# Kernel optimization log

Hardware: AMD Instinct MI355X
Metric: run time of the kernel (lower is better)

The kernel has to match this reference:

```python
import jax, jax.numpy as jnp
import numpy as np

D_MODEL = 1024
NUM_EXPERTS = 64
TOP_K = 2
TEMPERATURE = 1.0


def setup_inputs() -> dict:
    key = jax.random.key(0)
    k1, k2, k3, k4 = jax.random.split(key, 4)
    mh_output = jax.random.normal(k1, (8, 4096, D_MODEL), dtype=jnp.float32)
    noise = jax.random.normal(k2, (8, 4096, NUM_EXPERTS), dtype=jnp.float32)  # randn_like sample, externalized
    # nn.Linear weights: shape [out, in], init normal(0, 0.02); biases zero
    W_route = jax.random.normal(k3, (NUM_EXPERTS, D_MODEL), dtype=jnp.float32) * 0.02
    b_route = jnp.zeros((NUM_EXPERTS,), dtype=jnp.float32)
    W_noise = jax.random.normal(k4, (NUM_EXPERTS, D_MODEL), dtype=jnp.float32) * 0.02
    b_noise = jnp.zeros((NUM_EXPERTS,), dtype=jnp.float32)
    return {"mh_output": mh_output, "noise": noise, "W_route": W_route,
            "b_route": b_route, "W_noise": W_noise, "b_noise": b_noise}


def reference(mh_output, noise, W_route, b_route, W_noise, b_noise):
    # logits = topkroute_linear(mh_output); noise_logits = noise_linear(mh_output)
    logits = jnp.einsum('bsd,ed->bse', mh_output, W_route) + b_route
    noise_logits = jnp.einsum('bsd,ed->bse', mh_output, W_noise) + b_noise
    # noisy logits = logits + temperature * randn * softplus(noise_logits)
    noisy = logits + TEMPERATURE * noise * jax.nn.softplus(noise_logits)
    # top-k, scatter into -inf, softmax  ==  softmax over top-k values scattered into zeros
    top_vals, indices = jax.lax.top_k(noisy, TOP_K)          # [b, s, k]
    probs_k = jax.nn.softmax(top_vals, axis=-1)              # softmax(-inf elsewhere) -> 0 elsewhere
    one_hot = jax.nn.one_hot(indices, NUM_EXPERTS, dtype=noisy.dtype)  # [b, s, k, E]
    router_output = jnp.sum(one_hot * probs_k[..., None], axis=-2)     # [b, s, E]
    return router_output, indices
```

## Files before the change

### kernel.cpp

```cpp
#include <hip/hip_runtime.h>
#include <hip/hip_bf16.h>
#include <math.h>


#define T_TOKENS 32768
#define D_MODEL  1024
#define NE       64
#define NCOL     128
#define M_TILE   64
#define NCHUNK   32
#define CS_LD    68
#define OUT_IDX_BASE ((size_t)T_TOKENS * NE)
#define W_ELEMS  (NCOL * D_MODEL)

typedef short  bf16x8  __attribute__((ext_vector_type(8)));
typedef float  floatx4 __attribute__((ext_vector_type(4)));

__device__ __forceinline__ float softplus_f(float x) {
    return fmaxf(x, 0.f) + log1pf(expf(-fabsf(x)));
}

__device__ __forceinline__ void cvt8(const float4 a, const float4 b,
                                     int4* hi, int4* lo) {
    float v[8] = {a.x, a.y, a.z, a.w, b.x, b.y, b.z, b.w};
    int hw[4], lw[4];
    #pragma unroll
    for (int p = 0; p < 4; ++p) {
        float2 f2 = make_float2(v[2 * p], v[2 * p + 1]);
        __hip_bfloat162 h2 = __float22bfloat162_rn(f2);
        int u; __builtin_memcpy(&u, &h2, 4);
        float h0 = __uint_as_float(((unsigned)u) << 16);
        float h1 = __uint_as_float(((unsigned)u) & 0xFFFF0000u);
        float2 l2 = make_float2(v[2 * p] - h0, v[2 * p + 1] - h1);
        __hip_bfloat162 L2 = __float22bfloat162_rn(l2);
        int ul; __builtin_memcpy(&ul, &L2, 4);
        hw[p] = u; lw[p] = ul;
    }
    *hi = make_int4(hw[0], hw[1], hw[2], hw[3]);
    *lo = make_int4(lw[0], lw[1], lw[2], lw[3]);
}

__global__ __launch_bounds__(256) void prepack_w(
    const float* __restrict__ Wr, const float* __restrict__ Wn,
    short* __restrict__ Bh, short* __restrict__ Bl)
{
    int g   = blockIdx.x * 256 + threadIdx.x;
    int n   = g & 15;
    int kg  = (g >> 4) & 127;
    int t2  = g >> 11;
    int col = t2 * 16 + n;
    const float* src = (col < NE ? Wr + (size_t)col * D_MODEL
                                 : Wn + (size_t)(col - NE) * D_MODEL) + kg * 8;
    float4 a = *(const float4*)src;
    float4 b = *(const float4*)(src + 4);
    int4 hi, lo;
    cvt8(a, b, &hi, &lo);
    *(int4*)(Bh + (size_t)g * 8) = hi;
    *(int4*)(Bl + (size_t)g * 8) = lo;
}

__global__ __launch_bounds__(256, 2) void router_mfma(
    const float* __restrict__ A,
    const float* __restrict__ noise,
    const float* __restrict__ br,
    const float* __restrict__ bn,
    const short* __restrict__ Bh,
    const short* __restrict__ Bl,
    float* __restrict__ out)
{
    __shared__ __align__(16) short Ah[2][M_TILE * 32];
    __shared__ __align__(16) short Al[2][M_TILE * 32];
    __shared__ float Cs[M_TILE * CS_LD];
    __shared__ float s_p1[M_TILE], s_p2[M_TILE];
    __shared__ int   s_e1[M_TILE], s_e2[M_TILE];

    const int tid  = threadIdx.x;
    const int lane = tid & 63;
    const int wid  = tid >> 6;
    const int n16  = lane & 15;
    const int quad = lane >> 4;
    const int m0   = blockIdx.x * M_TILE;

    const int r  = tid & 63;
    const int kh = tid >> 6;
    const float* pA = A + (size_t)(m0 + r) * D_MODEL + kh * 8;
    const int sBase = (kh * M_TILE + r) * 8;

    const int bBaseR = ((wid * 128 + quad) * 16 + n16) * 8;
    const int bBaseN = (((4 + wid) * 128 + quad) * 16 + n16) * 8;

    floatx4 acc[4][2];
    #pragma unroll
    for (int i = 0; i < 4; ++i) { acc[i][0] = (floatx4)0.f; acc[i][1] = (floatx4)0.f; }

    {
        float4 a0 = *(const float4*)pA;
        float4 a1 = *(const float4*)(pA + 4);
        int4 hi, lo;
        cvt8(a0, a1, &hi, &lo);
        *(int4*)&Ah[0][sBase] = hi;
        *(int4*)&Al[0][sBase] = lo;
    }
    bf16x8 bhR, blR, bhN, blN;
    bhR = *(const bf16x8*)(Bh + bBaseR);
    blR = *(const bf16x8*)(Bl + bBaseR);
    bhN = *(const bf16x8*)(Bh + bBaseN);
    blN = *(const bf16x8*)(Bl + bBaseN);
    float4 aP1a = *(const float4*)(pA + 32), aP1b = *(const float4*)(pA + 36);
    float4 aP2a = *(const float4*)(pA + 64), aP2b = *(const float4*)(pA + 68);
    __syncthreads();

    for (int kc = 0; kc < NCHUNK; ++kc) {
        const int cur = kc & 1, nxt = cur ^ 1;

        float4 f0, f1;
        if (kc + 3 < NCHUNK) {
            f0 = *(const float4*)(pA + (kc + 3) * 32);
            f1 = *(const float4*)(pA + (kc + 3) * 32 + 4);
        }
        bf16x8 bhRn, blRn, bhNn, blNn;
        if (kc + 1 < NCHUNK) {
            int o = (kc + 1) * 512;
            bhRn = *(const bf16x8*)(Bh + bBaseR + o);
            blRn = *(const bf16x8*)(Bl + bBaseR + o);
            bhNn = *(const bf16x8*)(Bh + bBaseN + o);
            blNn = *(const bf16x8*)(Bl + bBaseN + o);
        }

        bf16x8 afh[4], afl[4];
        #pragma unroll
        for (int mf = 0; mf < 4; ++mf) {
            int g = (quad * M_TILE + mf * 16 + n16) * 8;
            afh[mf] = *(const bf16x8*)&Ah[cur][g];
            afl[mf] = *(const bf16x8*)&Al[cur][g];
        }

        if (kc + 1 < NCHUNK) {
            int4 hi, lo;
            cvt8(aP1a, aP1b, &hi, &lo);
            *(int4*)&Ah[nxt][sBase] = hi;
            *(int4*)&Al[nxt][sBase] = lo;
        }

        #pragma unroll
        for (int mf = 0; mf < 4; ++mf) {
            acc[mf][0] = __builtin_amdgcn_mfma_f32_16x16x32_bf16(afh[mf], bhR, acc[mf][0], 0, 0, 0);
            acc[mf][0] = __builtin_amdgcn_mfma_f32_16x16x32_bf16(afh[mf], blR, acc[mf][0], 0, 0, 0);
            acc[mf][0] = __builtin_amdgcn_mfma_f32_16x16x32_bf16(afl[mf], bhR, acc[mf][0], 0, 0, 0);
            acc[mf][1] = __builtin_amdgcn_mfma_f32_16x16x32_bf16(afh[mf], bhN, acc[mf][1], 0, 0, 0);
            acc[mf][1] = __builtin_amdgcn_mfma_f32_16x16x32_bf16(afh[mf], blN, acc[mf][1], 0, 0, 0);
            acc[mf][1] = __builtin_amdgcn_mfma_f32_16x16x32_bf16(afl[mf], blN == blN ? bhN : bhN, acc[mf][1], 0, 0, 0);
        }

        __syncthreads();

        aP1a = aP2a; aP1b = aP2b; aP2a = f0; aP2b = f1;
        bhR = bhRn; blR = blRn; bhN = bhNn; blN = blNn;
    }

    {
        int e = wid * 16 + n16;
        float brv = br[e], bnv = bn[e];
        #pragma unroll
        for (int mf = 0; mf < 4; ++mf)
            #pragma unroll
            for (int rr = 0; rr < 4; ++rr) {
                int t = mf * 16 + quad * 4 + rr;
                float nz    = noise[(size_t)(m0 + t) * NE + e];
                float route = acc[mf][0][rr] + brv;
                float nl    = acc[mf][1][rr] + bnv;
                Cs[t * CS_LD + e] = fmaf(nz, softplus_f(nl), route);
            }
    }
    __syncthreads();

    if (tid < M_TILE) {
        const int t = tid;
        float v1 = -INFINITY, v2 = -INFINITY;
        int e1 = 0, e2 = 0;
        #pragma unroll
        for (int e4 = 0; e4 < 16; ++e4) {
            float4 q = *(const float4*)&Cs[t * CS_LD + e4 * 4];
            float qa[4] = {q.x, q.y, q.z, q.w};
            #pragma unroll
            for (int c = 0; c < 4; ++c) {
                float v = qa[c];
                int e = e4 * 4 + c;
                if (v > v1) { v2 = v1; e2 = e1; v1 = v; e1 = e; }
                else if (v > v2) { v2 = v; e2 = e; }
            }
        }
        float ex = expf(v2 - v1);
        float denom = 1.f + ex;
        s_p1[t] = 1.f / denom;
        s_p2[t] = ex / denom;
        s_e1[t] = e1;
        s_e2[t] = e2;
        float2 iv = make_float2((float)e1, (float)e2);
        *(float2*)(out + OUT_IDX_BASE + (size_t)(m0 + t) * 2) = iv;
    }
    __syncthreads();

    #pragma unroll
    for (int i = 0; i < 4; ++i) {
        int gi = i * 256 + tid;
        int t  = gi >> 4;
        int e0 = (gi & 15) * 4;
        float p1 = s_p1[t], p2 = s_p2[t];
        int   e1 = s_e1[t], e2 = s_e2[t];
        float4 v;
        v.x = (e0 + 0 == e1) ? p1 : ((e0 + 0 == e2) ? p2 : 0.f);
        v.y = (e0 + 1 == e1) ? p1 : ((e0 + 1 == e2) ? p2 : 0.f);
        v.z = (e0 + 2 == e1) ? p1 : ((e0 + 2 == e2) ? p2 : 0.f);
        v.w = (e0 + 3 == e1) ? p1 : ((e0 + 3 == e2) ? p2 : 0.f);
        *(float4*)(out + (size_t)(m0 + t) * NE + e0) = v;
    }
}

extern "C" void kernel_launch(void* const* d_in, const int* in_sizes, int n_in,
                              void* d_out, int out_size, void* d_ws, size_t ws_size,
                              hipStream_t stream) {
    const float* A     = (const float*)d_in[0];
    const float* noise = (const float*)d_in[1];
    const float* Wr    = (const float*)d_in[2];
    const float* br    = (const float*)d_in[3];
    const float* Wn    = (const float*)d_in[4];
    const float* bn    = (const float*)d_in[5];
    float* out = (float*)d_out;

    short* Bh = (short*)d_ws;
    short* Bl = Bh + W_ELEMS;

    prepack_w<<<dim3(W_ELEMS / 8 / 256), dim3(256), 0, stream>>>(Wr, Wn, Bh, Bl);
    router_mfma<<<dim3(T_TOKENS / M_TILE), dim3(256), 0, stream>>>(A, noise, br, bn, Bh, Bl, out);
}
```

Baseline: 229.3 us.

## Load A fragments directly into registers, dropping LDS staging and loop barriers

Each wave now converts its own A rows from global memory straight into MFMA fragments instead of staging hi/lo bf16 tiles in shared memory. The block's warps are re-split into a 2x2 grid over tokens and columns, so each wave covers 32 tokens by 64 columns. This removes the per-chunk LDS writes, reads and __syncthreads, and drops the min-2-blocks launch bound. The cost is that each A element is loaded and converted by two waves, and more B fragments are held in registers, which raises register pressure and can lower occupancy.

```diff
diff --git a/kernel.cpp b/kernel.cpp
--- a/kernel.cpp
+++ b/kernel.cpp
@@ -20,8 +20,8 @@
     return fmaxf(x, 0.f) + log1pf(expf(-fabsf(x)));
 }
 
-__device__ __forceinline__ void cvt8(const float4 a, const float4 b,
-                                     int4* hi, int4* lo) {
+__device__ __forceinline__ void cvt8frag(const float4 a, const float4 b,
+                                         bf16x8* hi, bf16x8* lo) {
     float v[8] = {a.x, a.y, a.z, a.w, b.x, b.y, b.z, b.w};
     int hw[4], lw[4];
     #pragma unroll
@@ -36,8 +36,10 @@
         int ul; __builtin_memcpy(&ul, &L2, 4);
         hw[p] = u; lw[p] = ul;
     }
-    *hi = make_int4(hw[0], hw[1], hw[2], hw[3]);
-    *lo = make_int4(lw[0], lw[1], lw[2], lw[3]);
+    int4 hp = make_int4(hw[0], hw[1], hw[2], hw[3]);
+    int4 lp = make_int4(lw[0], lw[1], lw[2], lw[3]);
+    __builtin_memcpy(hi, &hp, 16);
+    __builtin_memcpy(lo, &lp, 16);
 }
 
 __global__ __launch_bounds__(256) void prepack_w(
@@ -53,13 +55,13 @@
                                  : Wn + (size_t)(col - NE) * D_MODEL) + kg * 8;
     float4 a = *(const float4*)src;
     float4 b = *(const float4*)(src + 4);
-    int4 hi, lo;
-    cvt8(a, b, &hi, &lo);
-    *(int4*)(Bh + (size_t)g * 8) = hi;
-    *(int4*)(Bl + (size_t)g * 8) = lo;
-}
-
-__global__ __launch_bounds__(256, 2) void router_mfma(
+    bf16x8 hi, lo;
+    cvt8frag(a, b, &hi, &lo);
+    *(bf16x8*)(Bh + (size_t)g * 8) = hi;
+    *(bf16x8*)(Bl + (size_t)g * 8) = lo;
+}
+
+__global__ __launch_bounds__(256) void router_mfma(
     const float* __restrict__ A,
     const float* __restrict__ noise,
     const float* __restrict__ br,
@@ -68,8 +70,6 @@
     const short* __restrict__ Bl,
     float* __restrict__ out)
 {
-    __shared__ __align__(16) short Ah[2][M_TILE * 32];
-    __shared__ __align__(16) short Al[2][M_TILE * 32];
     __shared__ float Cs[M_TILE * CS_LD];
     __shared__ float s_p1[M_TILE], s_p2[M_TILE];
     __shared__ int   s_e1[M_TILE], s_e2[M_TILE];
@@ -77,98 +77,101 @@
     const int tid  = threadIdx.x;
     const int lane = tid & 63;
     const int wid  = tid >> 6;
+    const int th   = wid >> 1;
+    const int wc   = wid & 1;
     const int n16  = lane & 15;
     const int quad = lane >> 4;
     const int m0   = blockIdx.x * M_TILE;
 
-    const int r  = tid & 63;
-    const int kh = tid >> 6;
-    const float* pA = A + (size_t)(m0 + r) * D_MODEL + kh * 8;
-    const int sBase = (kh * M_TILE + r) * 8;
-
-    const int bBaseR = ((wid * 128 + quad) * 16 + n16) * 8;
-    const int bBaseN = (((4 + wid) * 128 + quad) * 16 + n16) * 8;
-
-    floatx4 acc[4][2];
-    #pragma unroll
-    for (int i = 0; i < 4; ++i) { acc[i][0] = (floatx4)0.f; acc[i][1] = (floatx4)0.f; }
-
+    const float* pA0 = A + (size_t)(m0 + th * 32 + n16) * D_MODEL + quad * 8;
+    const float* pA1 = pA0 + (size_t)16 * D_MODEL;
+
+    int bBase[4];
+    #pragma unroll
+    for (int f = 0; f < 4; ++f) {
+        int ntile = (f < 2) ? (wc * 2 + f) : (4 + wc * 2 + (f - 2));
+        bBase[f] = ((ntile * 128 + quad) * 16 + n16) * 8;
+    }
+
+    floatx4 acc[2][4];
+    #pragma unroll
+    for (int mf = 0; mf < 2; ++mf)
+        #pragma unroll
+        for (int f = 0; f < 4; ++f) acc[mf][f] = (floatx4)0.f;
+
+    float4 r1[2][2], r2[2][2];
+    bf16x8 ah[2], al[2];
     {
-        float4 a0 = *(const float4*)pA;
-        float4 a1 = *(const float4*)(pA + 4);
-        int4 hi, lo;
-        cvt8(a0, a1, &hi, &lo);
-        *(int4*)&Ah[0][sBase] = hi;
-        *(int4*)&Al[0][sBase] = lo;
-    }
-    bf16x8 bhR, blR, bhN, blN;
-    bhR = *(const bf16x8*)(Bh + bBaseR);
-    blR = *(const bf16x8*)(Bl + bBaseR);
-    bhN = *(const bf16x8*)(Bh + bBaseN);
-    blN = *(const bf16x8*)(Bl + bBaseN);
-    float4 aP1a = *(const float4*)(pA + 32), aP1b = *(const float4*)(pA + 36);
-    float4 aP2a = *(const float4*)(pA + 64), aP2b = *(const float4*)(pA + 68);
-    __syncthreads();
+        float4 r0a0 = *(const float4*)(pA0);
+        float4 r0a1 = *(const float4*)(pA0 + 4);
+        float4 r0b0 = *(const float4*)(pA1);
+        float4 r0b1 = *(const float4*)(pA1 + 4);
+        r1[0][0] = *(const float4*)(pA0 + 32);  r1[0][1] = *(const float4*)(pA0 + 36);
+        r1[1][0] = *(const float4*)(pA1 + 32);  r1[1][1] = *(const float4*)(pA1 + 36);
+        r2[0][0] = *(const float4*)(pA0 + 64);  r2[0][1] = *(const float4*)(pA0 + 68);
+        r2[1][0] = *(const float4*)(pA1 + 64);  r2[1][1] = *(const float4*)(pA1 + 68);
+        cvt8frag(r0a0, r0a1, &ah[0], &al[0]);
+        cvt8frag(r0b0, r0b1, &ah[1], &al[1]);
+    }
+    bf16x8 bhc[4], blc[4];
+    #pragma unroll
+    for (int f = 0; f < 4; ++f) {
+        bhc[f] = *(const bf16x8*)(Bh + bBase[f]);
+        blc[f] = *(const bf16x8*)(Bl + bBase[f]);
+    }
 
     for (int kc = 0; kc < NCHUNK; ++kc) {
-        const int cur = kc & 1, nxt = cur ^ 1;
-
-        float4 f0, f1;
+        float4 r3[2][2];
         if (kc + 3 < NCHUNK) {
-            f0 = *(const float4*)(pA + (kc + 3) * 32);
-            f1 = *(const float4*)(pA + (kc + 3) * 32 + 4);
-        }
-        bf16x8 bhRn, blRn, bhNn, blNn;
+            const int o = (kc + 3) * 32;
+            r3[0][0] = *(const float4*)(pA0 + o);  r3[0][1] = *(const float4*)(pA0 + o + 4);
+            r3[1][0] = *(const float4*)(pA1 + o);  r3[1][1] = *(const float4*)(pA1 + o + 4);
+        }
+        bf16x8 bhn[4], bln[4];
         if (kc + 1 < NCHUNK) {
-            int o = (kc + 1) * 512;
-            bhRn = *(const bf16x8*)(Bh + bBaseR + o);
-            blRn = *(const bf16x8*)(Bl + bBaseR + o);
-            bhNn = *(const bf16x8*)(Bh + bBaseN + o);
-            blNn = *(const bf16x8*)(Bl + bBaseN + o);
-        }
-
-        bf16x8 afh[4], afl[4];
-        #pragma unroll
-        for (int mf = 0; mf < 4; ++mf) {
-            int g = (quad * M_TILE + mf * 16 + n16) * 8;
-            afh[mf] = *(const bf16x8*)&Ah[cur][g];
-            afl[mf] = *(const bf16x8*)&Al[cur][g];
-        }
+            const int o = (kc + 1) * 512;
+            #pragma unroll
+            for (int f = 0; f < 4; ++f) {
+                bhn[f] = *(const bf16x8*)(Bh + bBase[f] + o);
+                bln[f] = *(const bf16x8*)(Bl + bBase[f] + o);
+            }
+        }
+
+        #pragma unroll
+        for (int mf = 0; mf < 2; ++mf)
+            #pragma unroll
+            for (int f = 0; f < 4; ++f) {
+                acc[mf][f] = __builtin_amdgcn_mfma_f32_16x16x32_bf16(ah[mf], bhc[f], acc[mf][f], 0, 0, 0);
+                acc[mf][f] = __builtin_amdgcn_mfma_f32_16x16x32_bf16(ah[mf], blc[f], acc[mf][f], 0, 0, 0);
+                acc[mf][f] = __builtin_amdgcn_mfma_f32_16x16x32_bf16(al[mf], bhc[f], acc[mf][f], 0, 0, 0);
+            }
 
         if (kc + 1 < NCHUNK) {
-            int4 hi, lo;
-            cvt8(aP1a, aP1b, &hi, &lo);
-            *(int4*)&Ah[nxt][sBase] = hi;
-            *(int4*)&Al[nxt][sBase] = lo;
-        }
-
-        #pragma unroll
-        for (int mf = 0; mf < 4; ++mf) {
-            acc[mf][0] = __builtin_amdgcn_mfma_f32_16x16x32_bf16(afh[mf], bhR, acc[mf][0], 0, 0, 0);
-            acc[mf][0] = __builtin_amdgcn_mfma_f32_16x16x32_bf16(afh[mf], blR, acc[mf][0], 0, 0, 0);
-            acc[mf][0] = __builtin_amdgcn_mfma_f32_16x16x32_bf16(afl[mf], bhR, acc[mf][0], 0, 0, 0);
-            acc[mf][1] = __builtin_amdgcn_mfma_f32_16x16x32_bf16(afh[mf], bhN, acc[mf][1], 0, 0, 0);
-            acc[mf][1] = __builtin_amdgcn_mfma_f32_16x16x32_bf16(afh[mf], blN, acc[mf][1], 0, 0, 0);
-            acc[mf][1] = __builtin_amdgcn_mfma_f32_16x16x32_bf16(afl[mf], blN == blN ? bhN : bhN, acc[mf][1], 0, 0, 0);
-        }
-
-        __syncthreads();
-
-        aP1a = aP2a; aP1b = aP2b; aP2a = f0; aP2b = f1;
-        bhR = bhRn; blR = blRn; bhN = bhNn; blN = blNn;
-    }
-
-    {
-        int e = wid * 16 + n16;
+            cvt8frag(r1[0][0], r1[0][1], &ah[0], &al[0]);
+            cvt8frag(r1[1][0], r1[1][1], &ah[1], &al[1]);
+        }
+
+        #pragma unroll
+        for (int mf = 0; mf < 2; ++mf) {
+            r1[mf][0] = r2[mf][0]; r1[mf][1] = r2[mf][1];
+            r2[mf][0] = r3[mf][0]; r2[mf][1] = r3[mf][1];
+        }
+        #pragma unroll
+        for (int f = 0; f < 4; ++f) { bhc[f] = bhn[f]; blc[f] = bln[f]; }
+    }
+
+    #pragma unroll
+    for (int fi = 0; fi < 2; ++fi) {
+        int e = wc * 32 + fi * 16 + n16;
         float brv = br[e], bnv = bn[e];
         #pragma unroll
-        for (int mf = 0; mf < 4; ++mf)
+        for (int mf = 0; mf < 2; ++mf)
             #pragma unroll
             for (int rr = 0; rr < 4; ++rr) {
-                int t = mf * 16 + quad * 4 + rr;
+                int t = th * 32 + mf * 16 + quad * 4 + rr;
                 float nz    = noise[(size_t)(m0 + t) * NE + e];
-                float route = acc[mf][0][rr] + brv;
-                float nl    = acc[mf][1][rr] + bnv;
+                float route = acc[mf][fi]     [rr] + brv;
+                float nl    = acc[mf][fi + 2] [rr] + bnv;
                 Cs[t * CS_LD + e] = fmaf(nz, softplus_f(nl), route);
             }
     }
```

Measured after the change: 243.6 us. 6.2% more time.
